# Kernel optimization log

Hardware: AMD Instinct MI355X
Metric: run time of the kernel (lower is better)

Reference implementation:

```python
import jax, jax.numpy as jnp
import numpy as np

D_IN = 2
D_Q = 8
N_TOKEN = 512
FPD = 64            # fre_per_dim = (N_TOKEN*D_Q)**(1/D_IN)
FRE_UB = 10.0
FFN_MULT = 4
N_ATTN = 4
N_MLP = 2           # n_total_blocks - n_attn_blocks
B = 8192
EPS_LN = 1e-5
EPS_SIG = 1e-8


def _ln(x, g, b):
    m = jnp.mean(x, axis=-1, keepdims=True)
    v = jnp.var(x, axis=-1, keepdims=True)
    return (x - m) * jax.lax.rsqrt(v + EPS_LN) * g + b


def _rff_buffers():
    # freqs: linspace(0, fre_ub, FPD+1)[1:]
    f = jnp.linspace(0.0, FRE_UB, FPD + 1)[1:]
    # cartesian_prod(f, f): first factor varies slowest
    grid = jnp.stack(jnp.meshgrid(f, f, indexing='ij'), axis=-1).reshape(-1, D_IN)
    omega_raw = grid.reshape(N_TOKEN, D_Q, D_IN)
    G = omega_raw[..., -1]                                 # [T, d_q]
    f_min = G.min(axis=-1, keepdims=True)
    f_max = G.max(axis=-1, keepdims=True)
    G = (G - f_min) / (f_max - f_min + EPS_SIG) * 2.0 - 1.0
    omega = omega_raw * jnp.sqrt(jnp.asarray(2.0 / (D_Q * N_TOKEN), jnp.float32))
    phase = jnp.linspace(0.0, 2.0 * np.pi, N_TOKEN * D_Q).reshape(1, N_TOKEN, D_Q)
    return omega.astype(jnp.float32), G.astype(jnp.float32), phase.astype(jnp.float32)


def setup_inputs() -> dict:
    key = jax.random.key(0)
    ks = iter(jax.random.split(key, 64))
    T, F = N_TOKEN, FFN_MULT * N_TOKEN
    s = 0.02

    def w(shape):
        return (jax.random.normal(next(ks), shape, jnp.float32) * s)

    omega, G, phase = _rff_buffers()
    inp = {
        'x': jax.random.normal(next(ks), (B, D_IN), jnp.float32),
        'omega': omega, 'G': G, 'phase': phase,
        'l1_w': w((T, D_IN)), 'l1_b': jnp.zeros((T,), jnp.float32),
        # attention blocks (stacked over N_ATTN)
        'mu_w': w((N_ATTN, T, T)), 'mu_b': jnp.zeros((N_ATTN, T), jnp.float32),
        'sg_w': w((N_ATTN, T, T)), 'sg_b': jnp.zeros((N_ATTN, T), jnp.float32),
        'aln_q_g': jnp.ones((N_ATTN, T), jnp.float32), 'aln_q_b': jnp.zeros((N_ATTN, T), jnp.float32),
        'aln_f_g': jnp.ones((N_ATTN, T), jnp.float32), 'aln_f_b': jnp.zeros((N_ATTN, T), jnp.float32),
        'a_w1': w((N_ATTN, F, T)), 'a_b1': jnp.zeros((N_ATTN, F), jnp.float32),
        'a_w2': w((N_ATTN, T, F)), 'a_b2': jnp.zeros((N_ATTN, T), jnp.float32),
        # MLP blocks (stacked over N_MLP)
        'mln_g': jnp.ones((N_MLP, T), jnp.float32), 'mln_b': jnp.zeros((N_MLP, T), jnp.float32),
        'm_w1': w((N_MLP, F, T)), 'm_b1': jnp.zeros((N_MLP, F), jnp.float32),
        'm_w2': w((N_MLP, T, F)), 'm_b2': jnp.zeros((N_MLP, T), jnp.float32),
        'ro_w': w((1, T)), 'ro_b': jnp.zeros((1,), jnp.float32),
    }
    return inp


def reference(x, omega, G, phase, l1_w, l1_b, mu_w, mu_b, sg_w, sg_b,
              aln_q_g, aln_q_b, aln_f_g, aln_f_b, a_w1, a_b1, a_w2, a_b2,
              mln_g, mln_b, m_w1, m_b1, m_w2, m_b2, ro_w, ro_b):
    # RFF tokenizer: H[b,n,k] = cos(omega[n,k,:] . x[b,:] + phase)
    H = jnp.cos(jnp.einsum('nkd,bd->bnk', omega, x) + phase)   # [B,T,d_q]
    Q = jax.nn.silu(x @ l1_w.T + l1_b)                          # [B,T]
    for i in range(N_ATTN):
        q = _ln(Q, aln_q_g[i], aln_q_b[i])
        mu = jnp.tanh(q @ mu_w[i].T + mu_b[i])[..., None]       # [B,T,1]
        sig = (q @ sg_w[i].T + sg_b[i])[..., None]              # [B,T,1]
        # Gaussian kernelized pseudo-attention; G broadcasts [T,d_q] -> [B,T,d_q]
        S = jnp.exp(-0.5 * (G - mu) ** 2 / (sig * sig + EPS_SIG))
        Q = Q + jnp.sum(S * H, axis=-1)
        h = _ln(Q, aln_f_g[i], aln_f_b[i])
        Q = Q + jax.nn.silu(h @ a_w1[i].T + a_b1[i]) @ a_w2[i].T + a_b2[i]
    for i in range(N_MLP):
        h = _ln(Q, mln_g[i], mln_b[i])
        Q = Q + jax.nn.silu(h @ m_w1[i].T + m_b1[i]) @ m_w2[i].T + m_b2[i]
    out = jax.nn.silu(Q) @ ro_w.T + ro_b                        # [B,1]
    return out[:, 0]
```

## Files before the change

### kernel.cpp

```cpp
#include <hip/hip_runtime.h>
#include <cmath>

namespace {

constexpr int BB = 8192;
constexpr int TT = 512;
constexpr int FF = 2048;
constexpr float EPS_LN  = 1e-5f;
constexpr float EPS_SIG = 1e-8f;

typedef _Float16 half8 __attribute__((ext_vector_type(8)));
typedef _Float16 half4 __attribute__((ext_vector_type(4)));
typedef float f32x4 __attribute__((ext_vector_type(4)));

typedef __attribute__((address_space(1))) void gvoid_t;
typedef __attribute__((address_space(3))) void lvoid_t;

__device__ __forceinline__ void async16(void* lds, const void* g) {
    __builtin_amdgcn_global_load_lds((gvoid_t*)g, (lvoid_t*)lds, 16, 0, 0);
}

__device__ __forceinline__ float silu_f(float v) {
    return v / (1.0f + expf(-v));
}
__device__ __forceinline__ float silu_fast(float v) {
    return v * __builtin_amdgcn_rcpf(1.0f + __expf(-v));
}
__device__ __forceinline__ float tanh_fast(float v) {
    float t = __expf(2.0f * fminf(fmaxf(v, -10.0f), 10.0f));
    return (t - 1.0f) * __builtin_amdgcn_rcpf(t + 1.0f);
}

__global__ __launch_bounds__(256) void cvtall_kernel(
    const float* __restrict__ mu_w, const float* __restrict__ sg_w,
    const float* __restrict__ a_w1, const float* __restrict__ a_w2,
    const float* __restrict__ m_w1, const float* __restrict__ m_w2,
    _Float16* __restrict__ msw_hi, _Float16* __restrict__ msw_lo,
    _Float16* __restrict__ aw1, _Float16* __restrict__ aw2,
    _Float16* __restrict__ mw1, _Float16* __restrict__ mw2) {
    int i = (blockIdx.x * 256 + threadIdx.x) * 4;
    if (i < 2097152) {
        const float* s; int base, ii = i;
        if (i < 1048576) { s = mu_w; base = 0; }
        else             { s = sg_w; base = 262144; ii -= 1048576; }
        int dst = ((ii >> 18) << 19) + base + (ii & 262143);
        float4 v = *(const float4*)(s + ii);
        half4 h, l;
        h[0] = (_Float16)v.x; h[1] = (_Float16)v.y;
        h[2] = (_Float16)v.z; h[3] = (_Float16)v.w;
        l[0] = (_Float16)(v.x - (float)h[0]);
        l[1] = (_Float16)(v.y - (float)h[1]);
        l[2] = (_Float16)(v.z - (float)h[2]);
        l[3] = (_Float16)(v.w - (float)h[3]);
        *(half4*)(msw_hi + dst) = h;
        *(half4*)(msw_lo + dst) = l;
        return;
    }
    const float* s; _Float16* d; int ii;
    if      (i <  6291456) { s = a_w1; d = aw1; ii = i -  2097152; }
    else if (i < 10485760) { s = a_w2; d = aw2; ii = i -  6291456; }
    else if (i < 12582912) { s = m_w1; d = mw1; ii = i - 10485760; }
    else                   { s = m_w2; d = mw2; ii = i - 12582912; }
    float4 v = *(const float4*)(s + ii);
    half4 h;
    h[0] = (_Float16)v.x; h[1] = (_Float16)v.y;
    h[2] = (_Float16)v.z; h[3] = (_Float16)v.w;
    *(half4*)(d + ii) = h;
}

__global__ __launch_bounds__(512) void tokln_kernel(
    const float* __restrict__ x, const float* __restrict__ l1w,
    const float* __restrict__ l1b,
    const float* __restrict__ g, const float* __restrict__ bia,
    float* __restrict__ Q, _Float16* __restrict__ Y, _Float16* __restrict__ Ylo) {
    __shared__ float red[2][8];
    const int tid = threadIdx.x, b = blockIdx.x, t = tid;
    const float x0 = x[2 * b], x1 = x[2 * b + 1];
    float qn = silu_f(fmaf(x0, l1w[2 * t], fmaf(x1, l1w[2 * t + 1], l1b[t])));
    const size_t idx = (size_t)b * TT + t;
    Q[idx] = qn;
    const int wid = tid >> 6, lane = tid & 63;
    float s = qn;
    #pragma unroll
    for (int off = 32; off > 0; off >>= 1) s += __shfl_down(s, off);
    if (lane == 0) red[0][wid] = s;
    __syncthreads();
    float tot = 0.f;
    #pragma unroll
    for (int w = 0; w < 8; ++w) tot += red[0][w];
    float mean = tot * (1.0f / TT);
    float d = qn - mean;
    float ss = d * d;
    #pragma unroll
    for (int off = 32; off > 0; off >>= 1) ss += __shfl_down(ss, off);
    if (lane == 0) red[1][wid] = ss;
    __syncthreads();
    float vtot = 0.f;
    #pragma unroll
    for (int w = 0; w < 8; ++w) vtot += red[1][w];
    float rstd = rsqrtf(vtot * (1.0f / TT) + EPS_LN);
    float o = d * rstd * g[t] + bia[t];
    _Float16 hv = (_Float16)o;
    Y[idx] = hv;
    Ylo[idx] = (_Float16)(o - (float)hv);
}

template <bool LO>
__global__ __launch_bounds__(256) void ln_kernel(
    const float* __restrict__ X, const float* __restrict__ g,
    const float* __restrict__ bia, _Float16* __restrict__ Y,
    _Float16* __restrict__ Ylo) {
    int lane = threadIdx.x & 63;
    int row  = blockIdx.x * 4 + (threadIdx.x >> 6);
    const float* xr = X + (size_t)row * TT;
    float v[8];
    {
        float4 a = *(const float4*)(xr + lane * 8);
        float4 c = *(const float4*)(xr + lane * 8 + 4);
        v[0]=a.x; v[1]=a.y; v[2]=a.z; v[3]=a.w;
        v[4]=c.x; v[5]=c.y; v[6]=c.z; v[7]=c.w;
    }
    float s = 0.f;
    #pragma unroll
    for (int i = 0; i < 8; ++i) s += v[i];
    #pragma unroll
    for (int off = 32; off > 0; off >>= 1) s += __shfl_down(s, off);
    float mean = __shfl(s, 0) * (1.0f / TT);
    float ss = 0.f;
    #pragma unroll
    for (int i = 0; i < 8; ++i) { float d = v[i] - mean; ss = fmaf(d, d, ss); }
    #pragma unroll
    for (int off = 32; off > 0; off >>= 1) ss += __shfl_down(ss, off);
    float var  = __shfl(ss, 0) * (1.0f / TT);
    float rstd = rsqrtf(var + EPS_LN);
    half8 hv, lv;
    #pragma unroll
    for (int i = 0; i < 8; ++i) {
        int t = lane * 8 + i;
        float o = (v[i] - mean) * rstd * g[t] + bia[t];
        hv[i] = (_Float16)o;
        if (LO) lv[i] = (_Float16)(o - (float)hv[i]);
    }
    *(half8*)(Y + (size_t)row * TT + lane * 8) = hv;
    if (LO) *(half8*)(Ylo + (size_t)row * TT + lane * 8) = lv;
}

template <int BM, int BN, int BK, int WGM, int WGN, int NBUF, int MINW,
          bool SPLIT, int ACT, bool RESID, typename OutT>
__global__ __launch_bounds__(WGM * WGN * 64, MINW) void gemmdp_kernel(
    const _Float16* __restrict__ A, const _Float16* __restrict__ Alo,
    const _Float16* __restrict__ W, const _Float16* __restrict__ Wlo,
    const float* __restrict__ bias, const float* __restrict__ bias2,
    const float* __restrict__ R, OutT* __restrict__ C,
    int N, int K, int nsplit) {
    constexpr int THREADS = WGM * WGN * 64;
    constexpr int CPR  = BK / 8;
    constexpr int NS   = SPLIT ? 2 : 1;
    constexpr int D    = NBUF - 1;
    constexpr int CH_A = NS * BM * CPR;
    constexpr int CH_T = NS * (BM + BN) * CPR;
    constexpr int LPT  = CH_T / THREADS;
    static_assert(CH_T % THREADS == 0 && CH_A % THREADS == 0, "staging split");
    constexpr int ABUF = NS * BM * BK;
    constexpr int WBUF = NS * BN * BK;
    constexpr int WOFF = NBUF * ABUF;
    constexpr int WTM  = BM / WGM;
    constexpr int WTN  = BN / WGN;
    constexpr int MI   = WTM / 16;
    constexpr int NI   = WTN / 16;

    __shared__ alignas(16) _Float16 lds[NBUF * (ABUF + WBUF)];

    const int tid = threadIdx.x;
    const int m0  = blockIdx.x * BM;
    const int n0  = blockIdx.y * BN;

    const _Float16* Asrc[2] = {A, Alo};
    const _Float16* Wsrc[2] = {W, Wlo};

    const _Float16* gsrc[LPT];
    int off0[LPT], bstr[LPT];
    #pragma unroll
    for (int j = 0; j < LPT; ++j) {
        int idx = j * THREADS + tid;
        if (j * THREADS < CH_A) {
            int s   = idx / (BM * CPR);
            int rc  = idx % (BM * CPR);
            int row = rc / CPR, sl = rc % CPR;
            int src = sl ^ ((row >> 1) & (CPR - 1));
            gsrc[j] = Asrc[s] + (size_t)(m0 + row) * K + src * 8;
            off0[j] = (s * BM + row) * BK + sl * 8;
            bstr[j] = ABUF;
        } else {
            int i2  = idx - CH_A;
            int s   = i2 / (BN * CPR);
            int rc  = i2 % (BN * CPR);
            int row = rc / CPR, sl = rc % CPR;
            int src = sl ^ ((row >> 1) & (CPR - 1));
            gsrc[j] = Wsrc[s] + (size_t)(n0 + row) * K + src * 8;
            off0[j] = WOFF + (s * BN + row) * BK + sl * 8;
            bstr[j] = WBUF;
        }
    }

    auto stage = [&](int buf, int k0) {
        #pragma unroll
        for (int j = 0; j < LPT; ++j)
            async16(&lds[off0[j] + buf * bstr[j]], gsrc[j] + k0);
    };

    const int wid  = tid >> 6;
    const int wr   = wid / WGN;
    const int wc   = wid % WGN;
    const int lane = tid & 63;
    const int fr   = lane & 15;
    const int q    = lane >> 4;
    const int hxor = (fr >> 1) & (CPR - 1);

    const f32x4 vzero = {0.f, 0.f, 0.f, 0.f};
    f32x4 acc[MI][NI];
    #pragma unroll
    for (int mi = 0; mi < MI; ++mi)
        #pragma unroll
        for (int ni = 0; ni < NI; ++ni) acc[mi][ni] = vzero;

    auto body = [&](int buf) {
        const int da = buf * ABUF;
        const int dw = WOFF + buf * WBUF;
        #pragma unroll
        for (int ks = 0; ks < BK / 32; ++ks) {
            const int swz = ((ks * 4 + q) ^ hxor) * 8;
            half8 a[NS][MI], b[NS][NI];
            #pragma unroll
            for (int s = 0; s < NS; ++s) {
                #pragma unroll
                for (int mi = 0; mi < MI; ++mi)
                    a[s][mi] = *(const half8*)&lds[da + (s * BM + wr * WTM + mi * 16 + fr) * BK + swz];
                #pragma unroll
                for (int ni = 0; ni < NI; ++ni)
                    b[s][ni] = *(const half8*)&lds[dw + (s * BN + wc * WTN + ni * 16 + fr) * BK + swz];
            }
            __builtin_amdgcn_s_setprio(1);
            #pragma unroll
            for (int mi = 0; mi < MI; ++mi)
                #pragma unroll
                for (int ni = 0; ni < NI; ++ni)
                    acc[mi][ni] = __builtin_amdgcn_mfma_f32_16x16x32_f16(
                        a[0][mi], b[0][ni], acc[mi][ni], 0, 0, 0);
            if (SPLIT) {
                #pragma unroll
                for (int mi = 0; mi < MI; ++mi)
                    #pragma unroll
                    for (int ni = 0; ni < NI; ++ni)
                        acc[mi][ni] = __builtin_amdgcn_mfma_f32_16x16x32_f16(
                            a[1][mi], b[0][ni], acc[mi][ni], 0, 0, 0);
                #pragma unroll
                for (int mi = 0; mi < MI; ++mi)
                    #pragma unroll
                    for (int ni = 0; ni < NI; ++ni)
                        acc[mi][ni] = __builtin_amdgcn_mfma_f32_16x16x32_f16(
                            a[0][mi], b[1][ni], acc[mi][ni], 0, 0, 0);
            }
            __builtin_amdgcn_s_setprio(0);
        }
    };

    const int NK = K / BK;

    #pragma unroll
    for (int s = 0; s < D; ++s) stage(s, s * BK);

    int rbuf = 0, sbuf = D;
    for (int ki = 0; ki < NK - D; ++ki) {
        asm volatile("s_waitcnt vmcnt(%0)" :: "n"((D - 1) * LPT) : "memory");
        __builtin_amdgcn_s_barrier();
        asm volatile("" ::: "memory");
        stage(sbuf, (ki + D) * BK);
        sbuf = (sbuf + 1 == NBUF) ? 0 : sbuf + 1;
        body(rbuf);
        rbuf = (rbuf + 1 == NBUF) ? 0 : rbuf + 1;
    }
    if constexpr (D >= 4) {
        asm volatile("s_waitcnt vmcnt(%0)" :: "n"(3 * LPT) : "memory");
        __builtin_amdgcn_s_barrier();
        asm volatile("" ::: "memory");
        body(rbuf);
        rbuf = (rbuf + 1 == NBUF) ? 0 : rbuf + 1;
    }
    if constexpr (D >= 3) {
        asm volatile("s_waitcnt vmcnt(%0)" :: "n"(2 * LPT) : "memory");
        __builtin_amdgcn_s_barrier();
        asm volatile("" ::: "memory");
        body(rbuf);
        rbuf = (rbuf + 1 == NBUF) ? 0 : rbuf + 1;
    }
    if constexpr (D >= 2) {
        asm volatile("s_waitcnt vmcnt(%0)" :: "n"(1 * LPT) : "memory");
        __builtin_amdgcn_s_barrier();
        asm volatile("" ::: "memory");
        body(rbuf);
        rbuf = (rbuf + 1 == NBUF) ? 0 : rbuf + 1;
    }
    asm volatile("s_waitcnt vmcnt(0)" ::: "memory");
    __builtin_amdgcn_s_barrier();
    asm volatile("" ::: "memory");
    body(rbuf);

    const bool fh = (n0 < nsplit);
    const float* bp = fh ? bias : bias2;
    const int coff = fh ? 0 : nsplit;
    const int r0 = q * 4;
    #pragma unroll
    for (int mi = 0; mi < MI; ++mi) {
        #pragma unroll
        for (int ni = 0; ni < NI; ++ni) {
            const int col = n0 + wc * WTN + ni * 16 + fr;
            const float bv = bp[col - coff];
            #pragma unroll
            for (int r = 0; r < 4; ++r) {
                const int row = m0 + wr * WTM + mi * 16 + r0 + r;
                float v = acc[mi][ni][r] + bv;
                if (ACT == 1) v = silu_fast(v);
                if (ACT == 3 && fh) v = tanh_fast(v);
                if (RESID) v += R[(size_t)row * N + col];
                C[(size_t)row * N + col] = (OutT)v;
            }
        }
    }
}

__global__ __launch_bounds__(512) void attnln_kernel(
    float* __restrict__ Q, const float* __restrict__ MS,
    const float* __restrict__ x,
    const float* __restrict__ omega, const float* __restrict__ G,
    const float* __restrict__ phase,
    const float* __restrict__ g, const float* __restrict__ bia,
    _Float16* __restrict__ Y) {
    __shared__ float cs[8][516];
    __shared__ float gs[8][516];
    __shared__ float red[2][8];
    const int tid = threadIdx.x;
    const int b   = blockIdx.x;
    const float x0 = x[2 * b], x1 = x[2 * b + 1];
    #pragma unroll
    for (int it = 0; it < 8; ++it) {
        int j = it * 512 + tid;
        float2 om = *(const float2*)(omega + 2 * j);
        float arg = fmaf(om.x, x0, fmaf(om.y, x1, phase[j]));
        cs[j & 7][j >> 3] = __cosf(arg);
        gs[j & 7][j >> 3] = G[j];
    }
    __syncthreads();
    const int t = tid;
    float mu  = MS[(size_t)b * 1024 + t];
    float sig = MS[(size_t)b * 1024 + 512 + t];
    float inv = -0.5f * __builtin_amdgcn_rcpf(fmaf(sig, sig, EPS_SIG));
    float acc = 0.f;
    #pragma unroll
    for (int k = 0; k < 8; ++k) {
        float d = gs[k][t] - mu;
        acc = fmaf(__expf(d * d * inv), cs[k][t], acc);
    }
    const size_t idx = (size_t)b * TT + t;
    float qn = Q[idx] + acc;
    Q[idx] = qn;
    const int wid = tid >> 6, lane = tid & 63;
    float s = qn;
    #pragma unroll
    for (int off = 32; off > 0; off >>= 1) s += __shfl_down(s, off);
    if (lane == 0) red[0][wid] = s;
    __syncthreads();
    float tot = 0.f;
    #pragma unroll
    for (int w = 0; w < 8; ++w) tot += red[0][w];
    float mean = tot * (1.0f / TT);
    float d = qn - mean;
    float ss = d * d;
    #pragma unroll
    for (int off = 32; off > 0; off >>= 1) ss += __shfl_down(ss, off);
    if (lane == 0) red[1][wid] = ss;
    __syncthreads();
    float vtot = 0.f;
    #pragma unroll
    for (int w = 0; w < 8; ++w) vtot += red[1][w];
    float rstd = rsqrtf(vtot * (1.0f / TT) + EPS_LN);
    Y[idx] = (_Float16)(d * rstd * g[t] + bia[t]);
}

__global__ __launch_bounds__(256) void readout_kernel(
    const float* __restrict__ Q, const float* __restrict__ row_,
    const float* __restrict__ rob, float* __restrict__ out) {
    int lane = threadIdx.x & 63;
    int row  = blockIdx.x * 4 + (threadIdx.x >> 6);
    const float* qr = Q + (size_t)row * TT;
    float acc = 0.f;
    #pragma unroll
    for (int i = 0; i < 8; ++i) {
        int t = lane * 8 + i;
        acc = fmaf(silu_f(qr[t]), row_[t], acc);
    }
    #pragma unroll
    for (int off = 32; off > 0; off >>= 1) acc += __shfl_down(acc, off);
    if (lane == 0) out[row] = acc + rob[0];
}

}

extern "C" void kernel_launch(void* const* d_in, const int* in_sizes, int n_in,
                              void* d_out, int out_size, void* d_ws, size_t ws_size,
                              hipStream_t stream) {
    const float* x     = (const float*)d_in[0];
    const float* omega = (const float*)d_in[1];
    const float* G     = (const float*)d_in[2];
    const float* phase = (const float*)d_in[3];
    const float* l1_w  = (const float*)d_in[4];
    const float* l1_b  = (const float*)d_in[5];
    const float* mu_w  = (const float*)d_in[6];
    const float* mu_b  = (const float*)d_in[7];
    const float* sg_w  = (const float*)d_in[8];
    const float* sg_b  = (const float*)d_in[9];
    const float* alqg  = (const float*)d_in[10];
    const float* alqb  = (const float*)d_in[11];
    const float* alfg  = (const float*)d_in[12];
    const float* alfb  = (const float*)d_in[13];
    const float* a_w1  = (const float*)d_in[14];
    const float* a_b1  = (const float*)d_in[15];
    const float* a_w2  = (const float*)d_in[16];
    const float* a_b2  = (const float*)d_in[17];
    const float* mln_g = (const float*)d_in[18];
    const float* mln_b = (const float*)d_in[19];
    const float* m_w1  = (const float*)d_in[20];
    const float* m_b1  = (const float*)d_in[21];
    const float* m_w2  = (const float*)d_in[22];
    const float* m_b2  = (const float*)d_in[23];
    const float* ro_w  = (const float*)d_in[24];
    const float* ro_b  = (const float*)d_in[25];

    char* ws = (char*)d_ws;
    float*     Q    = (float*)ws;
    _Float16*  h_hi = (_Float16*)(ws + 16777216);
    _Float16*  h_lo = (_Float16*)(ws + 25165824);
    _Float16*  mid  = (_Float16*)(ws + 33554432);
    float*     MS   = (float*)(ws + 33554432);
    _Float16*  wbuf = (_Float16*)(ws + 67108864);

    _Float16* msw_hi = wbuf;
    _Float16* msw_lo = msw_hi + 2097152;
    _Float16* aw1    = msw_lo + 2097152;
    _Float16* aw2    = aw1 + 4194304;
    _Float16* mw1    = aw2 + 4194304;
    _Float16* mw2    = mw1 + 2097152;

    dim3 blk(256);
    const int BIG = 1 << 30;

    cvtall_kernel<<<14336, blk, 0, stream>>>(
        mu_w, sg_w, a_w1, a_w2, m_w1, m_w2,
        msw_hi, msw_lo, aw1, aw2, mw1, mw2);

    tokln_kernel<<<BB, dim3(512), 0, stream>>>(
        x, l1_w, l1_b, alqg, alqb, Q, h_hi, h_lo);

    for (int i = 0; i < 4; ++i) {
        if (i > 0)
            ln_kernel<true><<<BB / 4, blk, 0, stream>>>(
                Q, alqg + i * TT, alqb + i * TT, h_hi, h_lo);
        gemmdp_kernel<256, 128, 32, 4, 2, 3, 2, true, 3, false, float>
            <<<dim3(BB / 256, 1024 / 128), dim3(512), 0, stream>>>(
            h_hi, h_lo, msw_hi + (size_t)i * 524288, msw_lo + (size_t)i * 524288,
            mu_b + i * TT, sg_b + i * TT, nullptr, MS, 1024, TT, TT);
        attnln_kernel<<<BB, dim3(512), 0, stream>>>(
            Q, MS, x, omega, G, phase, alfg + i * TT, alfb + i * TT, h_hi);
        gemmdp_kernel<256, 128, 32, 4, 2, 3, 4, false, 1, false, _Float16>
            <<<dim3(BB / 256, FF / 128), dim3(512), 0, stream>>>(
            h_hi, nullptr, aw1 + (size_t)i * 1048576, nullptr,
            a_b1 + i * FF, a_b1 + i * FF, nullptr, mid, FF, TT, BIG);
        gemmdp_kernel<128, 128, 32, 2, 4, 5, 4, false, 0, true, float>
            <<<dim3(BB / 128, TT / 128), dim3(512), 0, stream>>>(
            mid, nullptr, aw2 + (size_t)i * 1048576, nullptr,
            a_b2 + i * TT, a_b2 + i * TT, Q, Q, TT, FF, BIG);
    }
    for (int i = 0; i < 2; ++i) {
        ln_kernel<false><<<BB / 4, blk, 0, stream>>>(
            Q, mln_g + i * TT, mln_b + i * TT, h_hi, nullptr);
        gemmdp_kernel<256, 128, 32, 4, 2, 3, 4, false, 1, false, _Float16>
            <<<dim3(BB / 256, FF / 128), dim3(512), 0, stream>>>(
            h_hi, nullptr, mw1 + (size_t)i * 1048576, nullptr,
            m_b1 + i * FF, m_b1 + i * FF, nullptr, mid, FF, TT, BIG);
        gemmdp_kernel<128, 128, 32, 2, 4, 5, 4, false, 0, true, float>
            <<<dim3(BB / 128, TT / 128), dim3(512), 0, stream>>>(
            mid, nullptr, mw2 + (size_t)i * 1048576, nullptr,
            m_b2 + i * TT, m_b2 + i * TT, Q, Q, TT, FF, BIG);
    }

    readout_kernel<<<BB / 4, blk, 0, stream>>>(Q, ro_w, ro_b, (float*)d_out);
}
```

Measured before the change: 737.9 us.

## Add dedicated 256x256 FFN-up GEMM kernel with 4-stage async pipeline

Adds a specialized gemm8p kernel for the FFN first projection (K=512, N=2048) using 256x256 tiles, 8 waves each computing 128x64, a 4-deep global_load_lds ring with explicit vmcnt waits, barriers interleaved per MFMA group and s_setprio around MFMA bursts. It is meant to raise arithmetic intensity per loaded byte and overlap staging with compute better than the generic 256x128 kernel. The cost is a larger register footprint (128 accumulator floats per thread), fewer blocks in the grid (256 instead of 512), and many barriers per K step.

New measurement: 723.8 us. Within noise of the previous version (-1.9%).

```diff
diff --git a/kernel.cpp b/kernel.cpp
--- a/kernel.cpp
+++ b/kernel.cpp
@@ -143,6 +143,110 @@
     }
     *(half8*)(Y + (size_t)row * TT + lane * 8) = hv;
     if (LO) *(half8*)(Ylo + (size_t)row * TT + lane * 8) = lv;
+}
+
+__global__ __launch_bounds__(512, 2) void gemm8p_kernel(
+    const _Float16* __restrict__ A, const _Float16* __restrict__ W,
+    const float* __restrict__ bias, _Float16* __restrict__ C, int N, int K) {
+    constexpr int BM = 256, BN = 256, BK = 32, NBUF = 4;
+    constexpr int ABUF = BM * BK;
+    constexpr int WOFF = NBUF * ABUF;
+
+    __shared__ alignas(16) _Float16 lds[2 * NBUF * ABUF];
+
+    const int tid = threadIdx.x;
+    const int m0  = blockIdx.x * BM;
+    const int n0  = blockIdx.y * BN;
+
+    const _Float16* gsrc[4];
+    int off0[4];
+    #pragma unroll
+    for (int j = 0; j < 4; ++j) {
+        int idx = j * 512 + tid;
+        int isW = idx >> 10;
+        int ch  = idx & 1023;
+        int row = ch >> 2, sl = ch & 3;
+        int src = sl ^ ((row >> 1) & 3);
+        gsrc[j] = (isW ? W + (size_t)(n0 + row) * K
+                       : A + (size_t)(m0 + row) * K) + src * 8;
+        off0[j] = isW * WOFF + row * BK + sl * 8;
+    }
+    auto stage1 = [&](int buf, int k0, int j) {
+        async16(&lds[off0[j] + buf * ABUF], gsrc[j] + k0);
+    };
+
+    const int wid  = tid >> 6;
+    const int wr   = wid >> 2;
+    const int wc   = wid & 3;
+    const int lane = tid & 63;
+    const int fr   = lane & 15;
+    const int q    = lane >> 4;
+    const int swz  = (q ^ ((fr >> 1) & 3)) * 8;
+
+    const _Float16* aB = &lds[(wr * 128 + fr) * BK + swz];
+    const _Float16* wB = &lds[WOFF + (wc * 64 + fr) * BK + swz];
+
+    f32x4 acc[8][4];
+    #pragma unroll
+    for (int mi = 0; mi < 8; ++mi)
+        #pragma unroll
+        for (int ni = 0; ni < 4; ++ni) acc[mi][ni] = {0.f, 0.f, 0.f, 0.f};
+
+    const int NK = K / BK;
+
+    #pragma unroll
+    for (int s = 0; s < 3; ++s)
+        #pragma unroll
+        for (int j = 0; j < 4; ++j) stage1(s, s * BK, j);
+
+    for (int t = 0; t < NK; ++t) {
+        const int d = (t & 3) * ABUF;
+        if (t < NK - 2)       { asm volatile("s_waitcnt vmcnt(8)" ::: "memory"); }
+        else if (t == NK - 2) { asm volatile("s_waitcnt vmcnt(4)" ::: "memory"); }
+        else                  { asm volatile("s_waitcnt vmcnt(0)" ::: "memory"); }
+        __builtin_amdgcn_s_barrier();
+        asm volatile("" ::: "memory");
+        const bool st = (t < NK - 3);
+        half8 b0 = *(const half8*)(wB + d);
+        half8 b1 = *(const half8*)(wB + d + 16 * BK);
+        half8 b2 = *(const half8*)(wB + d + 32 * BK);
+        half8 b3 = *(const half8*)(wB + d + 48 * BK);
+        #pragma unroll
+        for (int p = 0; p < 4; ++p) {
+            half8 a0 = *(const half8*)(aB + d + (2 * p)     * 16 * BK);
+            half8 a1 = *(const half8*)(aB + d + (2 * p + 1) * 16 * BK);
+            if (st) stage1((t + 3) & 3, (t + 3) * BK, p);
+            __builtin_amdgcn_s_barrier();
+            asm volatile("" ::: "memory");
+            __builtin_amdgcn_s_setprio(1);
+            acc[2*p][0]   = __builtin_amdgcn_mfma_f32_16x16x32_f16(a0, b0, acc[2*p][0],   0, 0, 0);
+            acc[2*p][1]   = __builtin_amdgcn_mfma_f32_16x16x32_f16(a0, b1, acc[2*p][1],   0, 0, 0);
+            acc[2*p][2]   = __builtin_amdgcn_mfma_f32_16x16x32_f16(a0, b2, acc[2*p][2],   0, 0, 0);
+            acc[2*p][3]   = __builtin_amdgcn_mfma_f32_16x16x32_f16(a0, b3, acc[2*p][3],   0, 0, 0);
+            acc[2*p+1][0] = __builtin_amdgcn_mfma_f32_16x16x32_f16(a1, b0, acc[2*p+1][0], 0, 0, 0);
+            acc[2*p+1][1] = __builtin_amdgcn_mfma_f32_16x16x32_f16(a1, b1, acc[2*p+1][1], 0, 0, 0);
+            acc[2*p+1][2] = __builtin_amdgcn_mfma_f32_16x16x32_f16(a1, b2, acc[2*p+1][2], 0, 0, 0);
+            acc[2*p+1][3] = __builtin_amdgcn_mfma_f32_16x16x32_f16(a1, b3, acc[2*p+1][3], 0, 0, 0);
+            __builtin_amdgcn_s_setprio(0);
+            __builtin_amdgcn_s_barrier();
+            asm volatile("" ::: "memory");
+        }
+    }
+
+    const int r0 = q * 4;
+    #pragma unroll
+    for (int mi = 0; mi < 8; ++mi) {
+        #pragma unroll
+        for (int ni = 0; ni < 4; ++ni) {
+            const int col = n0 + wc * 64 + ni * 16 + fr;
+            const float bv = bias[col];
+            #pragma unroll
+            for (int r = 0; r < 4; ++r) {
+                const int row = m0 + wr * 128 + mi * 16 + r0 + r;
+                C[(size_t)row * N + col] = (_Float16)silu_fast(acc[mi][ni][r] + bv);
+            }
+        }
+    }
 }
 
 template <int BM, int BN, int BK, int WGM, int WGN, int NBUF, int MINW,
@@ -471,10 +575,8 @@
             mu_b + i * TT, sg_b + i * TT, nullptr, MS, 1024, TT, TT);
         attnln_kernel<<<BB, dim3(512), 0, stream>>>(
             Q, MS, x, omega, G, phase, alfg + i * TT, alfb + i * TT, h_hi);
-        gemmdp_kernel<256, 128, 32, 4, 2, 3, 4, false, 1, false, _Float16>
-            <<<dim3(BB / 256, FF / 128), dim3(512), 0, stream>>>(
-            h_hi, nullptr, aw1 + (size_t)i * 1048576, nullptr,
-            a_b1 + i * FF, a_b1 + i * FF, nullptr, mid, FF, TT, BIG);
+        gemm8p_kernel<<<dim3(BB / 256, FF / 256), dim3(512), 0, stream>>>(
+            h_hi, aw1 + (size_t)i * 1048576, a_b1 + i * FF, mid, FF, TT);
         gemmdp_kernel<128, 128, 32, 2, 4, 5, 4, false, 0, true, float>
             <<<dim3(BB / 128, TT / 128), dim3(512), 0, stream>>>(
             mid, nullptr, aw2 + (size_t)i * 1048576, nullptr,
@@ -483,10 +585,8 @@
     for (int i = 0; i < 2; ++i) {
         ln_kernel<false><<<BB / 4, blk, 0, stream>>>(
             Q, mln_g + i * TT, mln_b + i * TT, h_hi, nullptr);
-        gemmdp_kernel<256, 128, 32, 4, 2, 3, 4, false, 1, false, _Float16>
-            <<<dim3(BB / 256, FF / 128), dim3(512), 0, stream>>>(
-            h_hi, nullptr, mw1 + (size_t)i * 1048576, nullptr,
-            m_b1 + i * FF, m_b1 + i * FF, nullptr, mid, FF, TT, BIG);
+        gemm8p_kernel<<<dim3(BB / 256, FF / 256), dim3(512), 0, stream>>>(
+            h_hi, mw1 + (size_t)i * 1048576, m_b1 + i * FF, mid, FF, TT);
         gemmdp_kernel<128, 128, 32, 2, 4, 5, 4, false, 0, true, float>
             <<<dim3(BB / 128, TT / 128), dim3(512), 0, stream>>>(
             mid, nullptr, mw2 + (size_t)i * 1048576, nullptr,
```
